# Kernel optimization log

Measured on AMD Instinct MI355X. Metric: run time of the kernel, lower is better.

## Reference

```python
import jax, jax.numpy as jnp
import numpy as np

N = 30000
E = 480000
VDIM = 512
HID = 32
EPS_BN = 1e-5
EPS_COS = 1e-8


def setup_inputs() -> dict:
    key = jax.random.key(0)
    ks = jax.random.split(key, 12)
    inp = {}
    inp["x"] = jax.random.normal(ks[0], (N, 2), dtype=jnp.float32)
    inp["visual"] = jax.random.normal(ks[1], (N, VDIM), dtype=jnp.float32)
    inp["edge_index"] = jax.random.randint(ks[2], (2, E), 0, N, dtype=jnp.int64)
    # input_mlp: Linear(2,32) -> BN(32) -> PReLU -> Dropout(0) -> Linear(32,32)
    inp["w1"] = jax.random.normal(ks[3], (HID, 2), dtype=jnp.float32) * 0.1
    inp["b1"] = jnp.zeros((HID,), dtype=jnp.float32)
    inp["gamma"] = jnp.ones((HID,), dtype=jnp.float32)
    inp["beta"] = jnp.zeros((HID,), dtype=jnp.float32)
    inp["prelu_a"] = jnp.asarray(0.25, dtype=jnp.float32)  # torch default: single shared slope
    inp["w2"] = jax.random.normal(ks[4], (HID, HID), dtype=jnp.float32) * 0.1
    inp["b2"] = jnp.zeros((HID,), dtype=jnp.float32)
    # CMCosConv(32, 32, 512): linear over cos-weighted mean aggregation
    inp["wc"] = jax.random.normal(ks[5], (HID, HID), dtype=jnp.float32) * 0.1
    inp["bc"] = jnp.zeros((HID,), dtype=jnp.float32)
    # gcn_projection_face: Linear(32,1)
    inp["wp"] = jax.random.normal(ks[6], (1, HID), dtype=jnp.float32) * 0.1
    inp["bp"] = jnp.zeros((1,), dtype=jnp.float32)
    return inp


def reference(x, visual, edge_index, w1, b1, gamma, beta, prelu_a, w2, b2, wc, bc, wp, bp):
    # ---- input_mlp ----
    h = x @ w1.T + b1  # [N,32]
    mu = jnp.mean(h, axis=0)
    var = jnp.mean((h - mu) ** 2, axis=0)  # biased, training-mode BN
    h = (h - mu) * jax.lax.rsqrt(var + EPS_BN) * gamma + beta
    h = jnp.where(h >= 0, h, prelu_a * h)  # PReLU, single slope
    h = h @ w2.T + b2  # [N,32]

    # ---- CMCosConv: edge weight = cos(visual_src, visual_dst); cos-weighted mean agg; linear ----
    vn = visual / jnp.maximum(jnp.linalg.norm(visual, axis=-1, keepdims=True), EPS_COS)  # [N,512]
    src = edge_index[0]
    dst = edge_index[1]
    w = jnp.sum(vn[src] * vn[dst], axis=-1)  # [E] cosine per edge (memory-bound gathers)
    msg = w[:, None] * h[src]  # [E,32]
    agg = jax.ops.segment_sum(msg, dst, num_segments=N)  # [N,32]
    deg = jax.ops.segment_sum(jnp.ones_like(w), dst, num_segments=N)  # [N]
    agg = agg / jnp.maximum(deg, 1.0)[:, None]  # mean aggregation
    hc = agg @ wc.T + bc  # [N,32]; conv_activation=None -> identity

    # ---- projection ----
    scores = (hc @ wp.T + bp).squeeze(-1)  # [N]
    return scores
```

## Files before the change

kernel.cpp:

```cpp
#include <hip/hip_runtime.h>
#include <hip/hip_fp16.h>
#include <math.h>

#define N_NODES 30000
#define E_EDGES 480000
#define VD      512
#define HID     32
#define BUCKET  3750
#define K1_BLOCKS 512

#define ACC_OFF  0
#define DEG_OFF  30000
#define SARR_OFF 60000
#define PART_OFF 90000
#define INV_OFF  92560
#define NV_BYTE_OFF 524288u

__device__ inline int edot4(unsigned int a, unsigned int b, int c) {
#if __has_builtin(__builtin_amdgcn_sdot4)
    return __builtin_amdgcn_sdot4((int)a, (int)b, (int)c, false);
#else
    int r = c;
    r += (int)(signed char)(a)       * (int)(signed char)(b);
    r += (int)(signed char)(a >> 8)  * (int)(signed char)(b >> 8);
    r += (int)(signed char)(a >> 16) * (int)(signed char)(b >> 16);
    r += (int)(signed char)(a >> 24) * (int)(signed char)(b >> 24);
    return r;
#endif
}

__device__ inline unsigned int pack4i8(float x0, float x1, float x2, float x3, float sc) {
    int q0 = (int)rintf(x0 * sc);
    int q1 = (int)rintf(x1 * sc);
    int q2 = (int)rintf(x2 * sc);
    int q3 = (int)rintf(x3 * sc);
    return (unsigned int)(q0 & 255) | ((unsigned int)(q1 & 255) << 8) |
           ((unsigned int)(q2 & 255) << 16) | ((unsigned int)(q3 & 255) << 24);
}

__global__ void __launch_bounds__(256) k1_prep(
        const float* __restrict__ x,
        const float* __restrict__ visual,
        float* __restrict__ ws, int i8mode) {
    const int t      = threadIdx.x;
    const int gid    = blockIdx.x * blockDim.x + t;
    const int stride = gridDim.x * blockDim.x;
    const int lane   = t & 63;

    for (int i = gid; i < 2 * N_NODES; i += stride) ws[i] = 0.f;

    {
        __shared__ float red[4][5];
        float s0 = 0.f, s1 = 0.f, s00 = 0.f, s11 = 0.f, s01 = 0.f;
        for (int i = gid; i < N_NODES; i += stride) {
            float2 v = ((const float2*)x)[i];
            s0  += v.x;       s1  += v.y;
            s00 += v.x * v.x; s11 += v.y * v.y;
            s01 += v.x * v.y;
        }
        for (int o = 32; o; o >>= 1) {
            s0  += __shfl_xor(s0,  o, 64);
            s1  += __shfl_xor(s1,  o, 64);
            s00 += __shfl_xor(s00, o, 64);
            s11 += __shfl_xor(s11, o, 64);
            s01 += __shfl_xor(s01, o, 64);
        }
        int wv = t >> 6;
        if (lane == 0) {
            red[wv][0] = s0; red[wv][1] = s1; red[wv][2] = s00;
            red[wv][3] = s11; red[wv][4] = s01;
        }
        __syncthreads();
        if (t < 5) {
            ws[PART_OFF + blockIdx.x * 5 + t] =
                red[0][t] + red[1][t] + red[2][t] + red[3][t];
        }
    }

    char*  nvis8 = (char*)ws + NV_BYTE_OFF;
    float* inv   = ws + INV_OFF;
    int wave  = gid >> 6;
    int nwave = stride >> 6;
    for (int node = wave; node < N_NODES; node += nwave) {
        const float4* row = (const float4*)(visual + (size_t)node * VD);
        float4 a = row[lane];
        float4 b = row[lane + 64];
        float p = a.x*a.x + a.y*a.y + a.z*a.z + a.w*a.w
                + b.x*b.x + b.y*b.y + b.z*b.z + b.w*b.w;
        float am = fmaxf(fmaxf(fmaxf(fabsf(a.x), fabsf(a.y)), fmaxf(fabsf(a.z), fabsf(a.w))),
                         fmaxf(fmaxf(fabsf(b.x), fabsf(b.y)), fmaxf(fabsf(b.z), fabsf(b.w))));
        for (int o = 32; o; o >>= 1) {
            p  += __shfl_xor(p, o, 64);
            am  = fmaxf(am, __shfl_xor(am, o, 64));
        }
        float r = 1.0f / fmaxf(sqrtf(p), 1e-8f);
        if (i8mode) {
            float vnmax = am * r;
            float qsc   = 127.0f / fmaxf(vnmax, 1e-20f);
            float rs    = r * qsc;
            uint2 q;
            q.x = pack4i8(a.x, a.y, a.z, a.w, rs);
            q.y = pack4i8(b.x, b.y, b.z, b.w, rs);
            uint2* orow = (uint2*)(nvis8 + (size_t)node * 512);
            orow[lane] = q;
            if (lane == 0) inv[node] = vnmax * (1.0f / 127.0f);
        } else if (lane == 0) {
            inv[node] = r;
        }
    }
}

__global__ void __launch_bounds__(256) k2_sarr(
        const float* __restrict__ x,
        const int* __restrict__ ei,
        const float* __restrict__ w1, const float* __restrict__ b1,
        const float* __restrict__ gamma, const float* __restrict__ beta,
        const float* __restrict__ prelu_a,
        const float* __restrict__ w2, const float* __restrict__ b2,
        const float* __restrict__ wc, const float* __restrict__ wp,
        const float* __restrict__ ws_ro,
        float* __restrict__ sarr,
        float* __restrict__ deg, int i8mode) {
    __shared__ float red[4][5];
    __shared__ float s_S[5];
    __shared__ float s_scale[HID], s_shift[HID], s_u[HID], s_w1a[HID], s_w1b[HID];
    __shared__ float s_wpc[HID];
    __shared__ float s_sb;
    const float* part = ws_ro + PART_OFF;
    const float* qs   = ws_ro + INV_OFF;
    const int t    = threadIdx.x;
    const int lane = t & 63;

    {
        float S[5] = {0.f, 0.f, 0.f, 0.f, 0.f};
        for (int j = t; j < K1_BLOCKS; j += 256) {
            #pragma unroll
            for (int c = 0; c < 5; ++c) S[c] += part[j * 5 + c];
        }
        #pragma unroll
        for (int c = 0; c < 5; ++c)
            for (int o = 32; o; o >>= 1) S[c] += __shfl_xor(S[c], o, 64);
        int wv = t >> 6;
        if (lane == 0) {
            #pragma unroll
            for (int c = 0; c < 5; ++c) red[wv][c] = S[c];
        }
        __syncthreads();
        if (t < 5) s_S[t] = red[0][t] + red[1][t] + red[2][t] + red[3][t];
        __syncthreads();
    }

    if (t < HID) {
        float wpck = 0.f;
        for (int j = 0; j < HID; ++j) wpck += wp[j] * wc[j * HID + t];
        s_wpc[t] = wpck;
        const float invN = 1.0f / (float)N_NODES;
        float m0  = s_S[0] * invN, m1 = s_S[1] * invN;
        float v0  = fmaxf(s_S[2] * invN - m0 * m0, 0.f);
        float v1  = fmaxf(s_S[3] * invN - m1 * m1, 0.f);
        float c01 = s_S[4] * invN - m0 * m1;
        float a0 = w1[2 * t], a1 = w1[2 * t + 1];
        float mean = a0 * m0 + a1 * m1 + b1[t];
        float var  = fmaxf(a0 * a0 * v0 + a1 * a1 * v1 + 2.f * a0 * a1 * c01, 0.f);
        float rs    = 1.0f / sqrtf(var + 1e-5f);
        float scale = gamma[t] * rs;
        s_scale[t] = scale;
        s_shift[t] = beta[t] - mean * scale;
        s_w1a[t] = a0; s_w1b[t] = a1;
    }
    __syncthreads();
    if (t < HID) {
        float uu = 0.f;
        for (int k = 0; k < HID; ++k) uu += s_wpc[k] * w2[k * HID + t];
        s_u[t] = uu;
    }
    if (t == 0) {
        float sb = 0.f;
        for (int k = 0; k < HID; ++k) sb += s_wpc[k] * b2[k];
        s_sb = sb;
    }
    __syncthreads();
    const float aslope = prelu_a[0];
    const float sb = s_sb;
    for (int i = blockIdx.x * blockDim.x + t; i < N_NODES; i += gridDim.x * blockDim.x) {
        float2 xv = ((const float2*)x)[i];
        float sacc = sb;
        #pragma unroll
        for (int c = 0; c < HID; ++c) {
            float h  = s_w1a[c] * xv.x + s_w1b[c] * xv.y + b1[c];
            float tt = h * s_scale[c] + s_shift[c];
            tt = tt >= 0.f ? tt : aslope * tt;
            sacc += tt * s_u[c];
        }
        sarr[i] = i8mode ? sacc * qs[i] : sacc;
    }

    for (int e = blockIdx.x * blockDim.x + t; e < E_EDGES; e += gridDim.x * blockDim.x) {
        atomicAdd(&deg[ei[E_EDGES + e]], 1.0f);
    }
}

__global__ void __launch_bounds__(256) k3_edge8(const int* __restrict__ ei,
                                                const float* __restrict__ ws_ro,
                                                float* __restrict__ acc,
                                                const float* __restrict__ sq) {
    const char* nvb = (const char*)ws_ro + NV_BYTE_OFF;
    const int lane = threadIdx.x & 63;
    const int sub  = lane & 7;
    const int g    = lane >> 3;
    const int r    = blockIdx.x & 7;
    const int q    = (blockIdx.x >> 3) * (blockDim.x >> 6) + (threadIdx.x >> 6);
    const int nq   = (gridDim.x >> 3) * (blockDim.x >> 6);
    const int nchunk = E_EDGES >> 6;

    for (int c = q; c < nchunk; c += nq) {
        int idx = (c << 6) + lane;
        int s = ei[idx];
        int d = ei[E_EDGES + idx];
        bool mine = (s / BUCKET == r);
        float mys = mine ? sq[s] : 0.f;
        unsigned long long m = __ballot(mine);
        while (m) {
            int j0 = __ffsll(m) - 1;  m &= m - 1;
            int cnt = 1;
            int j1 = j0, j2 = j0, j3 = j0, j4 = j0, j5 = j0, j6 = j0, j7 = j0;
            if (m) { j1 = __ffsll(m) - 1; m &= m - 1; cnt = 2; }
            if (m) { j2 = __ffsll(m) - 1; m &= m - 1; cnt = 3; }
            if (m) { j3 = __ffsll(m) - 1; m &= m - 1; cnt = 4; }
            if (m) { j4 = __ffsll(m) - 1; m &= m - 1; cnt = 5; }
            if (m) { j5 = __ffsll(m) - 1; m &= m - 1; cnt = 6; }
            if (m) { j6 = __ffsll(m) - 1; m &= m - 1; cnt = 7; }
            if (m) { j7 = __ffsll(m) - 1; m &= m - 1; cnt = 8; }

            int jsel = (g < 4) ? ((g < 2) ? (g == 0 ? j0 : j1) : (g == 2 ? j2 : j3))
                               : ((g < 6) ? (g == 4 ? j4 : j5) : (g == 6 ? j6 : j7));
            int   se = __shfl(s,   jsel, 64);
            int   de = __shfl(d,   jsel, 64);
            float sv = __shfl(mys, jsel, 64);

            const uint4* sa = (const uint4*)(nvb + ((size_t)se << 9)) + sub;
            const uint4* da = (const uint4*)(nvb + ((size_t)de << 9)) + sub;
            uint4 A0 = sa[0];
            uint4 B0 = da[0];
            uint4 A1 = sa[8];
            uint4 B1 = da[8];
            uint4 A2 = sa[16];
            uint4 B2 = da[16];
            uint4 A3 = sa[24];
            uint4 B3 = da[24];

            int p = 0;
            p = edot4(A0.x, B0.x, p);
            p = edot4(A0.y, B0.y, p);
            p = edot4(A0.z, B0.z, p);
            p = edot4(A0.w, B0.w, p);
            p = edot4(A1.x, B1.x, p);
            p = edot4(A1.y, B1.y, p);
            p = edot4(A1.z, B1.z, p);
            p = edot4(A1.w, B1.w, p);
            p = edot4(A2.x, B2.x, p);
            p = edot4(A2.y, B2.y, p);
            p = edot4(A2.z, B2.z, p);
            p = edot4(A2.w, B2.w, p);
            p = edot4(A3.x, B3.x, p);
            p = edot4(A3.y, B3.y, p);
            p = edot4(A3.z, B3.z, p);
            p = edot4(A3.w, B3.w, p);

            p += __shfl_xor(p, 4, 64);
            p += __shfl_xor(p, 2, 64);
            p += __shfl_xor(p, 1, 64);

            if (sub == 0 && g < cnt) {
                atomicAdd(&acc[de], (float)p * sv);
            }
        }
    }
}

__global__ void __launch_bounds__(256) k3_edge32(const int* __restrict__ ei,
                                                 const float* __restrict__ visual,
                                                 const float* __restrict__ inv,
                                                 const float* __restrict__ sarr,
                                                 float* __restrict__ acc) {
    int wave  = (blockIdx.x * blockDim.x + threadIdx.x) >> 6;
    int lane  = threadIdx.x & 63;
    int nwave = (gridDim.x * blockDim.x) >> 6;
    for (int e = wave; e < E_EDGES; e += nwave) {
        int s = ei[e];
        int d = ei[E_EDGES + e];
        const float4* ra = (const float4*)(visual + (size_t)s * VD);
        const float4* rb = (const float4*)(visual + (size_t)d * VD);
        float4 a0 = ra[lane];
        float4 b0 = rb[lane];
        float4 a1 = ra[lane + 64];
        float4 b1 = rb[lane + 64];
        float p = a0.x*b0.x + a0.y*b0.y + a0.z*b0.z + a0.w*b0.w
                + a1.x*b1.x + a1.y*b1.y + a1.z*b1.z + a1.w*b1.w;
        for (int o = 32; o; o >>= 1) p += __shfl_xor(p, o, 64);
        if (lane == 0) {
            float w = p * inv[s] * inv[d];
            atomicAdd(&acc[d], w * sarr[s]);
        }
    }
}

__global__ void k4_final(const float* __restrict__ acc, const float* __restrict__ deg,
                         const float* __restrict__ qs,
                         const float* __restrict__ bc, const float* __restrict__ wp,
                         const float* __restrict__ bp, float* __restrict__ out,
                         int n, int i8mode) {
    float K = bp[0];
    #pragma unroll
    for (int j = 0; j < HID; ++j) K += wp[j] * bc[j];
    for (int i = blockIdx.x * blockDim.x + threadIdx.x; i < n; i += gridDim.x * blockDim.x) {
        float a = acc[i];
        if (i8mode) a *= qs[i];
        out[i] = a / fmaxf(deg[i], 1.0f) + K;
    }
}

extern "C" void kernel_launch(void* const* d_in, const int* in_sizes, int n_in,
                              void* d_out, int out_size, void* d_ws, size_t ws_size,
                              hipStream_t stream) {
    const float* x       = (const float*)d_in[0];
    const float* visual  = (const float*)d_in[1];
    const int*   ei      = (const int*)  d_in[2];
    const float* w1      = (const float*)d_in[3];
    const float* b1      = (const float*)d_in[4];
    const float* gamma   = (const float*)d_in[5];
    const float* beta    = (const float*)d_in[6];
    const float* prelu_a = (const float*)d_in[7];
    const float* w2      = (const float*)d_in[8];
    const float* b2      = (const float*)d_in[9];
    const float* wc      = (const float*)d_in[10];
    const float* bc      = (const float*)d_in[11];
    const float* wp      = (const float*)d_in[12];
    const float* bp      = (const float*)d_in[13];
    float* out = (float*)d_out;

    float* ws   = (float*)d_ws;
    float* acc  = ws + ACC_OFF;
    float* deg  = ws + DEG_OFF;
    float* sarr = ws + SARR_OFF;
    float* inv  = ws + INV_OFF;

    bool i8ok = ws_size >= (size_t)NV_BYTE_OFF + (size_t)N_NODES * 512;

    k1_prep<<<K1_BLOCKS, 256, 0, stream>>>(x, visual, ws, i8ok ? 1 : 0);
    k2_sarr<<<512, 256, 0, stream>>>(x, ei, w1, b1, gamma, beta, prelu_a, w2, b2, wc, wp,
                                     ws, sarr, deg, i8ok ? 1 : 0);
    if (i8ok) {
        k3_edge8<<<4096, 256, 0, stream>>>(ei, ws, acc, sarr);
    } else {
        k3_edge32<<<4096, 256, 0, stream>>>(ei, visual, inv, sarr, acc);
    }
    k4_final<<<120, 256, 0, stream>>>(acc, deg, inv, bc, wp, bp, out, N_NODES, i8ok ? 1 : 0);
}
```

Before: 199.6 us.

## Process four nodes per wave in prep and fold degree count into edge kernel

The normalisation/quantisation loop in k1 now has each wave handle four visual rows at once, 16 lanes per row with eight float4 loads each, and a shorter shuffle reduction. Degree counting moves out of k2 into the edge kernels, where the lane that already updates acc also adds 1 to deg for the same destination. This drops a separate pass over the destination indices and its scattered atomics from k2, at the cost of an extra atomic per edge in the hot edge loop. N_NODES is a multiple of 4, so the grouped node indexing stays in bounds.

```diff
diff --git a/kernel.cpp b/kernel.cpp
--- a/kernel.cpp
+++ b/kernel.cpp
@@ -79,17 +79,30 @@
 
     char*  nvis8 = (char*)ws + NV_BYTE_OFF;
     float* inv   = ws + INV_OFF;
-    int wave  = gid >> 6;
-    int nwave = stride >> 6;
-    for (int node = wave; node < N_NODES; node += nwave) {
+    const int grp  = (lane >> 4);
+    const int sub  = lane & 15;
+    const int wave  = gid >> 6;
+    const int nwave = stride >> 6;
+    for (int base = wave * 4; base < N_NODES; base += nwave * 4) {
+        const int node = base + grp;
         const float4* row = (const float4*)(visual + (size_t)node * VD);
-        float4 a = row[lane];
-        float4 b = row[lane + 64];
-        float p = a.x*a.x + a.y*a.y + a.z*a.z + a.w*a.w
-                + b.x*b.x + b.y*b.y + b.z*b.z + b.w*b.w;
-        float am = fmaxf(fmaxf(fmaxf(fabsf(a.x), fabsf(a.y)), fmaxf(fabsf(a.z), fabsf(a.w))),
-                         fmaxf(fmaxf(fabsf(b.x), fabsf(b.y)), fmaxf(fabsf(b.z), fabsf(b.w))));
-        for (int o = 32; o; o >>= 1) {
+        float4 v0 = row[sub];
+        float4 v1 = row[sub + 16];
+        float4 v2 = row[sub + 32];
+        float4 v3 = row[sub + 48];
+        float4 v4 = row[sub + 64];
+        float4 v5 = row[sub + 80];
+        float4 v6 = row[sub + 96];
+        float4 v7 = row[sub + 112];
+        float p = 0.f, am = 0.f;
+        #define ACCUM(vv) \
+            p += vv.x*vv.x + vv.y*vv.y + vv.z*vv.z + vv.w*vv.w; \
+            am = fmaxf(am, fmaxf(fmaxf(fabsf(vv.x), fabsf(vv.y)), \
+                                 fmaxf(fabsf(vv.z), fabsf(vv.w))));
+        ACCUM(v0) ACCUM(v1) ACCUM(v2) ACCUM(v3)
+        ACCUM(v4) ACCUM(v5) ACCUM(v6) ACCUM(v7)
+        #undef ACCUM
+        for (int o = 8; o; o >>= 1) {
             p  += __shfl_xor(p, o, 64);
             am  = fmaxf(am, __shfl_xor(am, o, 64));
         }
@@ -98,13 +111,17 @@
             float vnmax = am * r;
             float qsc   = 127.0f / fmaxf(vnmax, 1e-20f);
             float rs    = r * qsc;
-            uint2 q;
-            q.x = pack4i8(a.x, a.y, a.z, a.w, rs);
-            q.y = pack4i8(b.x, b.y, b.z, b.w, rs);
-            uint2* orow = (uint2*)(nvis8 + (size_t)node * 512);
-            orow[lane] = q;
-            if (lane == 0) inv[node] = vnmax * (1.0f / 127.0f);
-        } else if (lane == 0) {
+            unsigned int* orow = (unsigned int*)(nvis8 + (size_t)node * 512);
+            orow[sub]       = pack4i8(v0.x, v0.y, v0.z, v0.w, rs);
+            orow[sub + 16]  = pack4i8(v1.x, v1.y, v1.z, v1.w, rs);
+            orow[sub + 32]  = pack4i8(v2.x, v2.y, v2.z, v2.w, rs);
+            orow[sub + 48]  = pack4i8(v3.x, v3.y, v3.z, v3.w, rs);
+            orow[sub + 64]  = pack4i8(v4.x, v4.y, v4.z, v4.w, rs);
+            orow[sub + 80]  = pack4i8(v5.x, v5.y, v5.z, v5.w, rs);
+            orow[sub + 96]  = pack4i8(v6.x, v6.y, v6.z, v6.w, rs);
+            orow[sub + 112] = pack4i8(v7.x, v7.y, v7.z, v7.w, rs);
+            if (sub == 0) inv[node] = vnmax * (1.0f / 127.0f);
+        } else if (sub == 0) {
             inv[node] = r;
         }
     }
@@ -112,15 +129,13 @@
 
 __global__ void __launch_bounds__(256) k2_sarr(
         const float* __restrict__ x,
-        const int* __restrict__ ei,
         const float* __restrict__ w1, const float* __restrict__ b1,
         const float* __restrict__ gamma, const float* __restrict__ beta,
         const float* __restrict__ prelu_a,
         const float* __restrict__ w2, const float* __restrict__ b2,
         const float* __restrict__ wc, const float* __restrict__ wp,
         const float* __restrict__ ws_ro,
-        float* __restrict__ sarr,
-        float* __restrict__ deg, int i8mode) {
+        float* __restrict__ sarr, int i8mode) {
     __shared__ float red[4][5];
     __shared__ float s_S[5];
     __shared__ float s_scale[HID], s_shift[HID], s_u[HID], s_w1a[HID], s_w1b[HID];
@@ -194,15 +209,12 @@
         }
         sarr[i] = i8mode ? sacc * qs[i] : sacc;
     }
-
-    for (int e = blockIdx.x * blockDim.x + t; e < E_EDGES; e += gridDim.x * blockDim.x) {
-        atomicAdd(&deg[ei[E_EDGES + e]], 1.0f);
-    }
 }
 
 __global__ void __launch_bounds__(256) k3_edge8(const int* __restrict__ ei,
                                                 const float* __restrict__ ws_ro,
                                                 float* __restrict__ acc,
+                                                float* __restrict__ deg,
                                                 const float* __restrict__ sq) {
     const char* nvb = (const char*)ws_ro + NV_BYTE_OFF;
     const int lane = threadIdx.x & 63;
@@ -273,6 +285,7 @@
 
             if (sub == 0 && g < cnt) {
                 atomicAdd(&acc[de], (float)p * sv);
+                atomicAdd(&deg[de], 1.0f);
             }
         }
     }
@@ -282,7 +295,8 @@
                                                  const float* __restrict__ visual,
                                                  const float* __restrict__ inv,
                                                  const float* __restrict__ sarr,
-                                                 float* __restrict__ acc) {
+                                                 float* __restrict__ acc,
+                                                 float* __restrict__ deg) {
     int wave  = (blockIdx.x * blockDim.x + threadIdx.x) >> 6;
     int lane  = threadIdx.x & 63;
     int nwave = (gridDim.x * blockDim.x) >> 6;
@@ -301,6 +315,7 @@
         if (lane == 0) {
             float w = p * inv[s] * inv[d];
             atomicAdd(&acc[d], w * sarr[s]);
+            atomicAdd(&deg[d], 1.0f);
         }
     }
 }
@@ -348,12 +363,12 @@
     bool i8ok = ws_size >= (size_t)NV_BYTE_OFF + (size_t)N_NODES * 512;
 
     k1_prep<<<K1_BLOCKS, 256, 0, stream>>>(x, visual, ws, i8ok ? 1 : 0);
-    k2_sarr<<<512, 256, 0, stream>>>(x, ei, w1, b1, gamma, beta, prelu_a, w2, b2, wc, wp,
-                                     ws, sarr, deg, i8ok ? 1 : 0);
+    k2_sarr<<<512, 256, 0, stream>>>(x, w1, b1, gamma, beta, prelu_a, w2, b2, wc, wp,
+                                     ws, sarr, i8ok ? 1 : 0);
     if (i8ok) {
-        k3_edge8<<<4096, 256, 0, stream>>>(ei, ws, acc, sarr);
+        k3_edge8<<<4096, 256, 0, stream>>>(ei, ws, acc, deg, sarr);
     } else {
-        k3_edge32<<<4096, 256, 0, stream>>>(ei, visual, inv, sarr, acc);
+        k3_edge32<<<4096, 256, 0, stream>>>(ei, visual, inv, sarr, acc, deg);
     }
     k4_final<<<120, 256, 0, stream>>>(acc, deg, inv, bc, wp, bp, out, N_NODES, i8ok ? 1 : 0);
 }
```

Result: faster. 185.0 us (-7.4%).
